# Optimization experiments

Hardware: AMD Instinct MI355X
Metric: run time of the kernel (lower is better)

Reference implementation:

```python
import math
import jax, jax.numpy as jnp
import numpy as np

B, S, D, H = 2, 2048, 2048, 16
HD = D // H
SCALE = 1.0 / math.sqrt(HD)


def setup_inputs() -> dict:
    key = jax.random.key(0)
    kx, kq, kk, kv, ko = jax.random.split(key, 5)
    w_std = 1.0 / math.sqrt(D)
    return {
        "x": jax.random.normal(kx, (B, S, D), jnp.float32),
        "Wq": jax.random.normal(kq, (D, D), jnp.float32) * w_std,
        "Wk": jax.random.normal(kk, (D, D), jnp.float32) * w_std,
        "Wv": jax.random.normal(kv, (D, D), jnp.float32) * w_std,
        "Wo": jax.random.normal(ko, (D, D), jnp.float32) * w_std,
        "attention_mask": jnp.ones((B, S), jnp.int32),
        "sliding_window": 512,
        "sink_tokens": 4,
    }


def reference(x, Wq, Wk, Wv, Wo, attention_mask, sliding_window, sink_tokens):
    b, s, d = x.shape
    # nn.Linear(bias=False): y = x @ W^T
    q = (x @ Wq.T).reshape(b, s, H, HD).transpose(0, 2, 1, 3)  # [b,h,s,hd]
    k = (x @ Wk.T).reshape(b, s, H, HD).transpose(0, 2, 1, 3)
    v = (x @ Wv.T).reshape(b, s, H, HD).transpose(0, 2, 1, 3)

    scores = jnp.einsum("bhqd,bhkd->bhqk", q, k) * SCALE  # [b,h,s,s]

    i = jnp.arange(s)[:, None]
    j = jnp.arange(s)[None, :]
    causal = j <= i
    window = (j >= i - sliding_window + 1) & (j <= i)
    # sink mask in the source fills [0:i+1] for every row (rows < sink_tokens
    # and rows >= sink_tokens alike), i.e. it is identical to the causal mask.
    sink = causal
    allowed = causal & window & sink  # [s,s]
    pad = (attention_mask != 0)[:, None, None, :]  # [b,1,1,s]
    scores = jnp.where(allowed[None, None] & pad, scores, -jnp.inf)

    attn = jax.nn.softmax(scores, axis=-1)
    out = jnp.einsum("bhqk,bhkd->bhqd", attn, v)  # [b,h,s,hd]
    out = out.transpose(0, 2, 1, 3).reshape(b, s, d)
    return out @ Wo.T
```

## Files before the change

kernel.cpp:

```cpp
#include <hip/hip_runtime.h>
#include <stdint.h>


typedef __attribute__((ext_vector_type(8))) short short8;
typedef __attribute__((ext_vector_type(4))) float f32x4;

#define DEV static __device__ __forceinline__

DEV unsigned short f2bf(float f) {
  unsigned u = __builtin_bit_cast(unsigned, f);
  u += 0x7fffu + ((u >> 16) & 1u);
  return (unsigned short)(u >> 16);
}

DEV void async16(const void* g, void* l) {
  __builtin_amdgcn_global_load_lds(
      (const __attribute__((address_space(1))) unsigned int*)g,
      (__attribute__((address_space(3))) unsigned int*)l, 16, 0, 0);
}

__global__ __launch_bounds__(256) void cast_all(
    const float* __restrict__ x, const float* __restrict__ Wq,
    const float* __restrict__ Wk, const float* __restrict__ Wv,
    const float* __restrict__ Wo, unsigned short* __restrict__ xb,
    unsigned short* __restrict__ wqkv, unsigned short* __restrict__ wob) {
  const int bid = blockIdx.x;
  const float* src;
  unsigned short* dst;
  int i;
  if (bid < 4096) {
    src = x; dst = xb; i = bid * 256 + threadIdx.x;
  } else if (bid < 6144) {
    src = Wq; dst = wqkv; i = (bid - 4096) * 256 + threadIdx.x;
  } else if (bid < 8192) {
    src = Wk; dst = wqkv + 4194304; i = (bid - 6144) * 256 + threadIdx.x;
  } else if (bid < 10240) {
    src = Wv; dst = wqkv + 8388608; i = (bid - 8192) * 256 + threadIdx.x;
  } else {
    src = Wo; dst = wob; i = (bid - 10240) * 256 + threadIdx.x;
  }
  const float4* s4 = (const float4*)src;
  float4 a = s4[2 * (size_t)i], b = s4[2 * (size_t)i + 1];
  short8 o;
  o[0] = (short)f2bf(a.x); o[1] = (short)f2bf(a.y);
  o[2] = (short)f2bf(a.z); o[3] = (short)f2bf(a.w);
  o[4] = (short)f2bf(b.x); o[5] = (short)f2bf(b.y);
  o[6] = (short)f2bf(b.z); o[7] = (short)f2bf(b.w);
  *(short8*)(dst + 8 * (size_t)i) = o;
}

constexpr int GK = 2048, GN = 2048;

template <bool STORE_BF16>
__global__ __launch_bounds__(256) void gemm_bt(
    const unsigned short* __restrict__ A, const unsigned short* __restrict__ B,
    void* __restrict__ Cout, size_t obuf_stride) {
  __shared__ short As[128 * 32];
  __shared__ short Bs[128 * 32];
  const int t = threadIdx.x;
  const int wave = t >> 6, lane = t & 63;
  const int row0 = blockIdx.x * 128;
  const int col0g = blockIdx.y * 128;
  const int nb = col0g >> 11, col0 = col0g & 2047;
  const int wrow = (wave >> 1) * 64, wcol = (wave & 1) * 64;

  f32x4 acc[4][4] = {};

  const int srow = wave * 16 + (lane >> 2);
  const int cg = (lane & 3) ^ (lane >> 4);
  const unsigned short* Ag0 = A + (size_t)(row0 + srow) * GK + cg * 8;
  const unsigned short* Ag1 = A + (size_t)(row0 + 64 + srow) * GK + cg * 8;
  const unsigned short* Bg0 = B + (size_t)(col0g + srow) * GK + cg * 8;
  const unsigned short* Bg1 = B + (size_t)(col0g + 64 + srow) * GK + cg * 8;
  char* lA0 = (char*)As + wave * 1024;
  char* lA1 = (char*)As + 4096 + wave * 1024;
  char* lB0 = (char*)Bs + wave * 1024;
  char* lB1 = (char*)Bs + 4096 + wave * 1024;

  const int quad = lane >> 4, l15 = lane & 15;
  const int cpos = quad ^ ((l15 >> 2) & 3);
  const short* ap[4];
  const short* bp[4];
#pragma unroll
  for (int i = 0; i < 4; ++i) {
    ap[i] = As + (wrow + i * 16 + l15) * 32 + cpos * 8;
    bp[i] = Bs + (wcol + i * 16 + l15) * 32 + cpos * 8;
  }

  for (int kk = 0; kk < GK; kk += 32) {
    async16(Ag0 + kk, lA0);
    async16(Ag1 + kk, lA1);
    async16(Bg0 + kk, lB0);
    async16(Bg1 + kk, lB1);
    __syncthreads();
    short8 af[4], bf[4];
#pragma unroll
    for (int i = 0; i < 4; ++i) af[i] = *(const short8*)ap[i];
#pragma unroll
    for (int i = 0; i < 4; ++i) bf[i] = *(const short8*)bp[i];
#pragma unroll
    for (int mi = 0; mi < 4; ++mi)
#pragma unroll
      for (int ni = 0; ni < 4; ++ni)
        acc[mi][ni] = __builtin_amdgcn_mfma_f32_16x16x32_bf16(
            af[mi], bf[ni], acc[mi][ni], 0, 0, 0);
    __syncthreads();
  }

#pragma unroll
  for (int mi = 0; mi < 4; ++mi)
#pragma unroll
    for (int ni = 0; ni < 4; ++ni)
#pragma unroll
      for (int r = 0; r < 4; ++r) {
        int row = row0 + wrow + mi * 16 + quad * 4 + r;
        int col = col0 + wcol + ni * 16 + l15;
        if (STORE_BF16)
          ((unsigned short*)Cout)[nb * obuf_stride + (size_t)row * GN + col] =
              f2bf(acc[mi][ni][r]);
        else
          ((float*)Cout)[nb * obuf_stride + (size_t)row * GN + col] =
              acc[mi][ni][r];
      }
}

__global__ __launch_bounds__(256) void transpose_v(
    const unsigned short* __restrict__ vb, unsigned short* __restrict__ vtb) {
  __shared__ unsigned short tile[64][72];
  const int s0 = blockIdx.x * 64, d0 = blockIdx.y * 64, b = blockIdx.z;
  const int tid = threadIdx.x;
  const int c8 = tid & 7;
#pragma unroll
  for (int i = 0; i < 2; ++i) {
    int row = i * 32 + (tid >> 3);
    uint4 v = *(const uint4*)(vb + (size_t)(b * 2048 + s0 + row) * 2048 + d0 + c8 * 8);
    *(uint4*)&tile[row][c8 * 8] = v;
  }
  __syncthreads();
#pragma unroll
  for (int i = 0; i < 2; ++i) {
    int dr = i * 32 + (tid >> 3);
    short8 sv;
#pragma unroll
    for (int j = 0; j < 8; ++j) sv[j] = (short)tile[c8 * 8 + j][dr];
    int d = d0 + dr;
    int h = d >> 7, hd = d & 127;
    *(short8*)(vtb + ((size_t)(b * 16 + h) * 128 + hd) * 2048 + s0 + c8 * 8) = sv;
  }
}

__global__ __launch_bounds__(256, 3) void attn_mfma(
    const unsigned short* __restrict__ Qm, const unsigned short* __restrict__ Km,
    const unsigned short* __restrict__ Vt, unsigned short* __restrict__ Om,
    const int* __restrict__ amask, const int* __restrict__ winp) {
  constexpr int S = 2048, D = 2048, HD = 128;
  const float SCALE = 0.08838834764831845f;

  __shared__ short Ks[64 * 128];
  __shared__ short Vts[128 * 64];
  __shared__ short Ps[4][16 * 64];

  const int t = threadIdx.x, w = t >> 6, lane = t & 63;
  const int quad = lane >> 4, l15 = lane & 15;
  const int l7 = l15 & 7;
  const int f = blockIdx.x;
  const int qt = f >> 5, g = f & 31;
  const int h = g & 15, b = g >> 4;
  const int qi0 = qt * 64;
  const int win = winp[0];

  short8 qf[4];
  {
    const unsigned short* qp =
        Qm + (size_t)(b * S + qi0 + w * 16 + l15) * D + h * HD + quad * 8;
#pragma unroll
    for (int kc = 0; kc < 4; ++kc) qf[kc] = *(const short8*)(qp + kc * 32);
  }

  f32x4 o[8] = {};
  float m_r[4], l_r[4];
#pragma unroll
  for (int r = 0; r < 4; ++r) { m_r[r] = -1e30f; l_r[r] = 0.f; }

  int lowj = qi0 - win + 1;
  if (lowj < 0) lowj = 0;
  const int jt0 = lowj >> 6;

  const int krow = lane >> 4, kpos = lane & 15;
  const int vrow = lane >> 3, vpos = lane & 7;

  for (int jt = jt0; jt <= qt; ++jt) {
    const int j0 = jt * 64;
    __syncthreads();
#pragma unroll
    for (int ii = 0; ii < 4; ++ii) {
      int row = ii * 16 + w * 4 + krow;
      int c = kpos ^ (row & 7);
      async16(Km + (size_t)(b * S + j0 + row) * D + h * HD + c * 8,
              (char*)Ks + (ii * 16 + w * 4) * 256);
    }
#pragma unroll
    for (int ii = 0; ii < 4; ++ii) {
      int row = ii * 32 + w * 8 + vrow;
      int c = vpos ^ (row & 7);
      async16(Vt + ((size_t)(b * 16 + h) * 128 + row) * S + j0 + c * 8,
              (char*)Vts + (ii * 32 + w * 8) * 128);
    }
    __syncthreads();

    f32x4 sS[4];
#pragma unroll
    for (int ni = 0; ni < 4; ++ni) {
      f32x4 acc = {0.f, 0.f, 0.f, 0.f};
#pragma unroll
      for (int kc = 0; kc < 4; ++kc) {
        int pos = (kc * 4 + quad) ^ l7;
        short8 bk = *(const short8*)&Ks[(ni * 16 + l15) * 128 + pos * 8];
        acc = __builtin_amdgcn_mfma_f32_16x16x32_bf16(qf[kc], bk, acc, 0, 0, 0);
      }
      sS[ni] = acc;
    }

    float sv[4][4];
    int amv[4];
#pragma unroll
    for (int ni = 0; ni < 4; ++ni) amv[ni] = amask[b * S + j0 + ni * 16 + l15];
#pragma unroll
    for (int ni = 0; ni < 4; ++ni)
#pragma unroll
      for (int r = 0; r < 4; ++r) {
        int gi = qi0 + w * 16 + quad * 4 + r;
        int gj = j0 + ni * 16 + l15;
        bool ok = (gj <= gi) && (gj >= gi - win + 1) && (amv[ni] != 0);
        sv[ni][r] = ok ? sS[ni][r] * SCALE : -1e30f;
      }
    float alpha[4], mnew[4];
#pragma unroll
    for (int r = 0; r < 4; ++r) {
      float mx = fmaxf(fmaxf(sv[0][r], sv[1][r]), fmaxf(sv[2][r], sv[3][r]));
      mx = fmaxf(mx, __shfl_xor(mx, 1));
      mx = fmaxf(mx, __shfl_xor(mx, 2));
      mx = fmaxf(mx, __shfl_xor(mx, 4));
      mx = fmaxf(mx, __shfl_xor(mx, 8));
      float mn = fmaxf(m_r[r], mx);
      alpha[r] = __expf(m_r[r] - mn);
      m_r[r] = mn;
      mnew[r] = mn;
    }
    float rs[4] = {0.f, 0.f, 0.f, 0.f};
#pragma unroll
    for (int ni = 0; ni < 4; ++ni)
#pragma unroll
      for (int r = 0; r < 4; ++r) {
        float p = (sv[ni][r] > -1e29f) ? __expf(sv[ni][r] - mnew[r]) : 0.f;
        sv[ni][r] = p;
        rs[r] += p;
      }
#pragma unroll
    for (int r = 0; r < 4; ++r) {
      float s = rs[r];
      s += __shfl_xor(s, 1);
      s += __shfl_xor(s, 2);
      s += __shfl_xor(s, 4);
      s += __shfl_xor(s, 8);
      l_r[r] = l_r[r] * alpha[r] + s;
    }
#pragma unroll
    for (int ni = 0; ni < 4; ++ni)
#pragma unroll
      for (int r = 0; r < 4; ++r) {
        int row = quad * 4 + r;
        int col = ni * 16 + l15;
        int pos = (col >> 3) ^ (row & 7);
        Ps[w][row * 64 + pos * 8 + (col & 7)] = (short)f2bf(sv[ni][r]);
      }
#pragma unroll
    for (int ni2 = 0; ni2 < 8; ++ni2)
#pragma unroll
      for (int r = 0; r < 4; ++r) o[ni2][r] *= alpha[r];

    __asm__ __volatile__("s_waitcnt lgkmcnt(0)" ::: "memory");

    short8 aP[2];
#pragma unroll
    for (int kc2 = 0; kc2 < 2; ++kc2) {
      int pos = (kc2 * 4 + quad) ^ l7;
      aP[kc2] = *(const short8*)&Ps[w][l15 * 64 + pos * 8];
    }
#pragma unroll
    for (int ni2 = 0; ni2 < 8; ++ni2) {
#pragma unroll
      for (int kc2 = 0; kc2 < 2; ++kc2) {
        int pos = (kc2 * 4 + quad) ^ l7;
        short8 bv = *(const short8*)&Vts[(ni2 * 16 + l15) * 64 + pos * 8];
        o[ni2] = __builtin_amdgcn_mfma_f32_16x16x32_bf16(aP[kc2], bv, o[ni2], 0, 0, 0);
      }
    }
  }

  float inv[4];
#pragma unroll
  for (int r = 0; r < 4; ++r) inv[r] = 1.f / l_r[r];
#pragma unroll
  for (int ni2 = 0; ni2 < 8; ++ni2)
#pragma unroll
    for (int r = 0; r < 4; ++r) {
      int row = qi0 + w * 16 + quad * 4 + r;
      Om[(size_t)(b * S + row) * D + h * HD + ni2 * 16 + l15] =
          f2bf(o[ni2][r] * inv[r]);
    }
}

extern "C" void kernel_launch(void* const* d_in, const int* in_sizes, int n_in,
                              void* d_out, int out_size, void* d_ws,
                              size_t ws_size, hipStream_t stream) {
  (void)in_sizes; (void)n_in; (void)out_size; (void)ws_size;
  const float* x  = (const float*)d_in[0];
  const float* Wq = (const float*)d_in[1];
  const float* Wk = (const float*)d_in[2];
  const float* Wv = (const float*)d_in[3];
  const float* Wo = (const float*)d_in[4];
  const int* am   = (const int*)d_in[5];
  const int* win  = (const int*)d_in[6];

  char* ws = (char*)d_ws;
  unsigned short* xb   = (unsigned short*)(ws + 0);
  unsigned short* vtb  = (unsigned short*)(ws + 0);
  unsigned short* wqkv = (unsigned short*)(ws + 16777216);
  unsigned short* wob  = (unsigned short*)(ws + 41943040);
  unsigned short* qb   = (unsigned short*)(ws + 50331648);
  unsigned short* kb   = (unsigned short*)(ws + 67108864);
  unsigned short* vb   = (unsigned short*)(ws + 83886080);
  unsigned short* ab   = (unsigned short*)(ws + 100663296);

  cast_all<<<dim3(12288), dim3(256), 0, stream>>>(x, Wq, Wk, Wv, Wo, xb, wqkv, wob);

  gemm_bt<true><<<dim3(32, 48), dim3(256), 0, stream>>>(xb, wqkv, qb, 8388608);

  transpose_v<<<dim3(32, 32, 2), dim3(256), 0, stream>>>(vb, vtb);

  attn_mfma<<<dim3(1024), dim3(256), 0, stream>>>(qb, kb, vtb, ab, am, win);

  gemm_bt<false><<<dim3(32, 16), dim3(256), 0, stream>>>(ab, wob, d_out, 0);
}
```

Baseline: 371.6 us.

## Fuse V transpose into QKV GEMM epilogue and reshape attention grid

The QKV projection GEMM now writes the V output directly in transposed [b, h*128+d, s] layout from its epilogue, which removes the separate transpose_v kernel and its extra read/write of V. The attention kernel now uses a 3D grid (qtile, head, batch) instead of a flattened index, which changes block scheduling order. Its launch bounds hint goes from 3 to 4 blocks per SM. The transposed stores are scattered 8-byte writes, so they may coalesce poorly, and the higher occupancy hint may cause register spills.

```diff
diff --git a/kernel.cpp b/kernel.cpp
--- a/kernel.cpp
+++ b/kernel.cpp
@@ -3,6 +3,7 @@
 
 
 typedef __attribute__((ext_vector_type(8))) short short8;
+typedef __attribute__((ext_vector_type(4))) short short4v;
 typedef __attribute__((ext_vector_type(4))) float f32x4;
 
 #define DEV static __device__ __forceinline__
@@ -51,10 +52,11 @@
 
 constexpr int GK = 2048, GN = 2048;
 
-template <bool STORE_BF16>
+template <bool STORE_BF16, bool TRANSPOSE_V>
 __global__ __launch_bounds__(256) void gemm_bt(
     const unsigned short* __restrict__ A, const unsigned short* __restrict__ B,
-    void* __restrict__ Cout, size_t obuf_stride) {
+    void* __restrict__ Cout, size_t obuf_stride,
+    unsigned short* __restrict__ Vtout) {
   __shared__ short As[128 * 32];
   __shared__ short Bs[128 * 32];
   const int t = threadIdx.x;
@@ -107,6 +109,22 @@
     __syncthreads();
   }
 
+  if (TRANSPOSE_V && nb == 2) {
+    const int bb = row0 >> 11;
+    const int sbase = (row0 & 2047) + wrow + quad * 4;
+#pragma unroll
+    for (int mi = 0; mi < 4; ++mi)
+#pragma unroll
+      for (int ni = 0; ni < 4; ++ni) {
+        int col = col0 + wcol + ni * 16 + l15;
+        short4v ov;
+#pragma unroll
+        for (int r = 0; r < 4; ++r) ov[r] = (short)f2bf(acc[mi][ni][r]);
+        *(short4v*)&Vtout[((size_t)(bb * 2048 + col)) * 2048 + sbase + mi * 16] = ov;
+      }
+    return;
+  }
+
 #pragma unroll
   for (int mi = 0; mi < 4; ++mi)
 #pragma unroll
@@ -124,32 +142,7 @@
       }
 }
 
-__global__ __launch_bounds__(256) void transpose_v(
-    const unsigned short* __restrict__ vb, unsigned short* __restrict__ vtb) {
-  __shared__ unsigned short tile[64][72];
-  const int s0 = blockIdx.x * 64, d0 = blockIdx.y * 64, b = blockIdx.z;
-  const int tid = threadIdx.x;
-  const int c8 = tid & 7;
-#pragma unroll
-  for (int i = 0; i < 2; ++i) {
-    int row = i * 32 + (tid >> 3);
-    uint4 v = *(const uint4*)(vb + (size_t)(b * 2048 + s0 + row) * 2048 + d0 + c8 * 8);
-    *(uint4*)&tile[row][c8 * 8] = v;
-  }
-  __syncthreads();
-#pragma unroll
-  for (int i = 0; i < 2; ++i) {
-    int dr = i * 32 + (tid >> 3);
-    short8 sv;
-#pragma unroll
-    for (int j = 0; j < 8; ++j) sv[j] = (short)tile[c8 * 8 + j][dr];
-    int d = d0 + dr;
-    int h = d >> 7, hd = d & 127;
-    *(short8*)(vtb + ((size_t)(b * 16 + h) * 128 + hd) * 2048 + s0 + c8 * 8) = sv;
-  }
-}
-
-__global__ __launch_bounds__(256, 3) void attn_mfma(
+__global__ __launch_bounds__(256, 4) void attn_mfma(
     const unsigned short* __restrict__ Qm, const unsigned short* __restrict__ Km,
     const unsigned short* __restrict__ Vt, unsigned short* __restrict__ Om,
     const int* __restrict__ amask, const int* __restrict__ winp) {
@@ -163,9 +156,7 @@
   const int t = threadIdx.x, w = t >> 6, lane = t & 63;
   const int quad = lane >> 4, l15 = lane & 15;
   const int l7 = l15 & 7;
-  const int f = blockIdx.x;
-  const int qt = f >> 5, g = f & 31;
-  const int h = g & 15, b = g >> 4;
+  const int qt = blockIdx.x, h = blockIdx.y, b = blockIdx.z;
   const int qi0 = qt * 64;
   const int win = winp[0];
 
@@ -203,7 +194,7 @@
     for (int ii = 0; ii < 4; ++ii) {
       int row = ii * 32 + w * 8 + vrow;
       int c = vpos ^ (row & 7);
-      async16(Vt + ((size_t)(b * 16 + h) * 128 + row) * S + j0 + c * 8,
+      async16(Vt + ((size_t)(b * 2048 + h * 128 + row)) * S + j0 + c * 8,
               (char*)Vts + (ii * 32 + w * 8) * 128);
     }
     __syncthreads();
@@ -325,21 +316,20 @@
 
   char* ws = (char*)d_ws;
   unsigned short* xb   = (unsigned short*)(ws + 0);
-  unsigned short* vtb  = (unsigned short*)(ws + 0);
   unsigned short* wqkv = (unsigned short*)(ws + 16777216);
   unsigned short* wob  = (unsigned short*)(ws + 41943040);
   unsigned short* qb   = (unsigned short*)(ws + 50331648);
   unsigned short* kb   = (unsigned short*)(ws + 67108864);
-  unsigned short* vb   = (unsigned short*)(ws + 83886080);
+  unsigned short* vtb  = (unsigned short*)(ws + 83886080);
   unsigned short* ab   = (unsigned short*)(ws + 100663296);
 
   cast_all<<<dim3(12288), dim3(256), 0, stream>>>(x, Wq, Wk, Wv, Wo, xb, wqkv, wob);
 
-  gemm_bt<true><<<dim3(32, 48), dim3(256), 0, stream>>>(xb, wqkv, qb, 8388608);
-
-  transpose_v<<<dim3(32, 32, 2), dim3(256), 0, stream>>>(vb, vtb);
-
-  attn_mfma<<<dim3(1024), dim3(256), 0, stream>>>(qb, kb, vtb, ab, am, win);
-
-  gemm_bt<false><<<dim3(32, 16), dim3(256), 0, stream>>>(ab, wob, d_out, 0);
-}
+  gemm_bt<true, true><<<dim3(32, 48), dim3(256), 0, stream>>>(
+      xb, wqkv, qb, 8388608, vtb);
+
+  attn_mfma<<<dim3(32, 16, 2), dim3(256), 0, stream>>>(qb, kb, vtb, ab, am, win);
+
+  gemm_bt<false, false><<<dim3(32, 16), dim3(256), 0, stream>>>(
+      ab, wob, d_out, 0, nullptr);
+}
```

New measurement: 412.9 us. +11.1%, slower.
